# Optimization experiments

Measured on AMD Instinct MI355X. Metric: run time of the kernel, lower is better.

Reference implementation:

```python
import jax, jax.numpy as jnp
import numpy as np

NUM_ITERATIONS = 3
EPS = 1e-08

def squash(s, axis=-1):
    norm = jnp.linalg.norm(s, axis=axis, keepdims=True)
    scale = norm ** 2 / (1 + norm ** 2)
    return scale * s / (norm + EPS)

def setup_inputs() -> dict:
    key = jax.random.key(0)
    k1, k2 = jax.random.split(key)
    B, C, M, O, I = 256, 1152, 8, 16, 8
    u = jax.random.normal(k1, (B, C, I), dtype=jnp.float32)
    W = jax.random.normal(k2, (C, M, O, I), dtype=jnp.float32)
    return {"u": u, "W": W}

def reference(u, W):
    B, C, I = u.shape
    M, O = W.shape[1], W.shape[2]
    # u_hat: [B, C, M, O] -- predicted output capsule vectors
    u_hat = jnp.einsum('cmoi,bci->bcmo', W, u)
    b = jnp.zeros((B, C, M), dtype=u.dtype)
    v = None
    for r in range(NUM_ITERATIONS):
        c = jax.nn.softmax(b, axis=2)  # softmax over emotion dim
        s = jnp.einsum('bcm,bcmo->bmo', c, u_hat)
        v = squash(s)  # [B, M, O]
        if r < NUM_ITERATIONS - 1:
            uv = jnp.einsum('bcmo,bmo->bcm', u_hat, v)
            b = b + uv
    return v
```

## Files before the change

kernel.cpp:

```cpp
#include <hip/hip_runtime.h>

#define B_SZ 256
#define C_SZ 1152
#define MO   128
#define CSPL 32
#define CRNG (C_SZ / CSPL)
#define CAPS_EPS 1e-8f

struct alignas(8) H4 { _Float16 h[4]; };
union PK2 { unsigned int u32; _Float16 h[2]; };

__global__ __launch_bounds__(256) void caps_uhat(
    const float* __restrict__ u,
    const float* __restrict__ W,
    unsigned int* __restrict__ uhat)
{
    const int bid = blockIdx.x;
    const int c   = (bid & 7) * 144 + (bid >> 3);
    const int l   = threadIdx.x & 63;
    const int wv  = __builtin_amdgcn_readfirstlane(threadIdx.x >> 6);

    const float4* wp =
        reinterpret_cast<const float4*>(W + (size_t)c * 1024) + l * 4;
    const float4 wa = wp[0], wb = wp[1], wc4 = wp[2], wd = wp[3];

    unsigned int* ub = uhat + (size_t)c * B_SZ * 64 + l;
    const int b0 = wv * 64;

    for (int bb = 0; bb < 64; bb += 8) {
#pragma unroll
        for (int k = 0; k < 8; ++k) {
            const int b = b0 + bb + k;
            const float4* up = reinterpret_cast<const float4*>(
                u + ((size_t)b * C_SZ + c) * 8);
            const float4 u0 = up[0], u1 = up[1];
            float h0 = wa.x*u0.x + wa.y*u0.y + wa.z*u0.z + wa.w*u0.w
                     + wb.x*u1.x + wb.y*u1.y + wb.z*u1.z + wb.w*u1.w;
            float h1 = wc4.x*u0.x + wc4.y*u0.y + wc4.z*u0.z + wc4.w*u0.w
                     + wd.x*u1.x + wd.y*u1.y + wd.z*u1.z + wd.w*u1.w;
            PK2 pk;
            pk.h[0] = (_Float16)h0;
            pk.h[1] = (_Float16)h1;
            ub[(size_t)b * 64] = pk.u32;
        }
    }
}

__global__ __launch_bounds__(128) void caps_vcalc(
    const float* __restrict__ part_in,
    const float* __restrict__ addv,
    float* __restrict__ vout)
{
    const int b = blockIdx.x, t = threadIdx.x;
    float s = 0.f;
#pragma unroll
    for (int k = 0; k < CSPL; ++k)
        s += part_in[((size_t)k * B_SZ + b) * MO + t];
    float n2 = s * s;
    n2 += __shfl_xor(n2, 1);
    n2 += __shfl_xor(n2, 2);
    n2 += __shfl_xor(n2, 4);
    n2 += __shfl_xor(n2, 8);
    float norm = sqrtf(n2);
    float v = (n2 / (1.f + n2)) * s / (norm + CAPS_EPS);
    if (addv) v += addv[(size_t)b * MO + t];
    vout[(size_t)b * MO + t] = v;
}

template <bool UNIF>
__global__ __launch_bounds__(256) void caps_route(
    const H4* __restrict__ uhat,
    const float* __restrict__ vbuf,
    float* __restrict__ part_out)
{
    const int bt  = blockIdx.x & 31;
    const int csp = blockIdx.x >> 5;
    const int tid = threadIdx.x;
    const int g   = tid >> 5;
    const int l   = tid & 31;
    const int b   = bt * 8 + g;
    const int mo4 = l * 4;

    float4 v4 = make_float4(0.f, 0.f, 0.f, 0.f);
    if (!UNIF)
        v4 = *reinterpret_cast<const float4*>(vbuf + (size_t)b * MO + mo4);
    float acc[4] = {0.f, 0.f, 0.f, 0.f};

    const int cbeg = csp * CRNG, cend = cbeg + CRNG;
    const H4* base = uhat + (size_t)b * 32 + l;

    H4 r0 = base[(size_t)cbeg * B_SZ * 32];
    H4 r1 = base[(size_t)(cbeg + 1) * B_SZ * 32];

    for (int c = cbeg; c < cend; c += 2) {
        H4 n0 = r0, n1 = r1;
        if (c + 2 < cend) {
            n0 = base[(size_t)(c + 2) * B_SZ * 32];
            n1 = base[(size_t)(c + 3) * B_SZ * 32];
        }
#pragma unroll
        for (int q = 0; q < 2; ++q) {
            H4 r = q ? r1 : r0;
            float uh0 = (float)r.h[0], uh1 = (float)r.h[1];
            float uh2 = (float)r.h[2], uh3 = (float)r.h[3];
            float cw;
            if (UNIF) {
                cw = 0.125f;
            } else {
                float uv = uh0 * v4.x + uh1 * v4.y + uh2 * v4.z + uh3 * v4.w;
                uv += __shfl_xor(uv, 1);
                uv += __shfl_xor(uv, 2);
                float mx = fmaxf(uv, __shfl_xor(uv, 4));
                mx = fmaxf(mx, __shfl_xor(mx, 8));
                mx = fmaxf(mx, __shfl_xor(mx, 16));
                float e = expf(uv - mx);
                float den = e;
                den += __shfl_xor(den, 4);
                den += __shfl_xor(den, 8);
                den += __shfl_xor(den, 16);
                cw = e / den;
            }
            acc[0] = fmaf(cw, uh0, acc[0]);
            acc[1] = fmaf(cw, uh1, acc[1]);
            acc[2] = fmaf(cw, uh2, acc[2]);
            acc[3] = fmaf(cw, uh3, acc[3]);
        }
        r0 = n0; r1 = n1;
    }
    *reinterpret_cast<float4*>(part_out + ((size_t)csp * B_SZ + b) * MO + mo4) =
        make_float4(acc[0], acc[1], acc[2], acc[3]);
}

template <int R>
__global__ __launch_bounds__(256) void caps_small(
    const float* __restrict__ u, const float* __restrict__ W,
    const float* __restrict__ s_in, const float* __restrict__ v0_in,
    float* __restrict__ s_out, float* __restrict__ v0_out,
    float* __restrict__ out)
{
    const int b = blockIdx.x, tid = threadIdx.x;
    __shared__ float sh_v[8][17];
    __shared__ float sh_part[256][17];

    if (R >= 1) {
        if (tid < 128) {
            float val = s_in[b * 128 + tid];
            float n2 = val * val;
            n2 += __shfl_xor(n2, 1); n2 += __shfl_xor(n2, 2);
            n2 += __shfl_xor(n2, 4); n2 += __shfl_xor(n2, 8);
            float norm = sqrtf(n2);
            float v = (n2 / (1.f + n2)) * val / (norm + CAPS_EPS);
            int m = tid >> 4, o = tid & 15;
            if (R == 1) { v0_out[b * 128 + tid] = v; sh_v[m][o] = v; }
            else        { sh_v[m][o] = v + v0_in[b * 128 + tid]; }
        }
        __syncthreads();
    }
    const int c_local = tid >> 3, m = tid & 7;
    float s_acc[16];
#pragma unroll
    for (int o = 0; o < 16; ++o) s_acc[o] = 0.f;
    for (int cc = 0; cc < C_SZ; cc += 32) {
        const int c = cc + c_local;
        const float4* up = reinterpret_cast<const float4*>(
            u + (size_t)(b * C_SZ + c) * 8);
        float4 u0 = up[0], u1 = up[1];
        float u8[8] = {u0.x, u0.y, u0.z, u0.w, u1.x, u1.y, u1.z, u1.w};
        float uh[16];
        const float4* wp = reinterpret_cast<const float4*>(
            W + (size_t)((c * 8 + m) * 16) * 8);
#pragma unroll
        for (int o = 0; o < 16; ++o) {
            float4 w0 = wp[o * 2], w1 = wp[o * 2 + 1];
            uh[o] = w0.x * u8[0] + w0.y * u8[1] + w0.z * u8[2] + w0.w * u8[3] +
                    w1.x * u8[4] + w1.y * u8[5] + w1.z * u8[6] + w1.w * u8[7];
        }
        float cw;
        if (R == 0) cw = 0.125f;
        else {
            float uv = 0.f;
#pragma unroll
            for (int o = 0; o < 16; ++o) uv = fmaf(uh[o], sh_v[m][o], uv);
            float mx = uv;
            mx = fmaxf(mx, __shfl_xor(mx, 1));
            mx = fmaxf(mx, __shfl_xor(mx, 2));
            mx = fmaxf(mx, __shfl_xor(mx, 4));
            float e = expf(uv - mx);
            float den = e;
            den += __shfl_xor(den, 1); den += __shfl_xor(den, 2);
            den += __shfl_xor(den, 4);
            cw = e / den;
        }
#pragma unroll
        for (int o = 0; o < 16; ++o) s_acc[o] = fmaf(cw, uh[o], s_acc[o]);
    }
#pragma unroll
    for (int o = 0; o < 16; ++o) sh_part[tid][o] = s_acc[o];
    __syncthreads();
    if (tid < 128) {
        const int m2 = tid >> 4, o2 = tid & 15;
        float s = 0.f;
#pragma unroll
        for (int gg = 0; gg < 32; ++gg) s += sh_part[gg * 8 + m2][o2];
        if (R < 2) s_out[b * 128 + tid] = s;
        else {
            float n2 = s * s;
            n2 += __shfl_xor(n2, 1); n2 += __shfl_xor(n2, 2);
            n2 += __shfl_xor(n2, 4); n2 += __shfl_xor(n2, 8);
            float norm = sqrtf(n2);
            out[b * 128 + tid] = (n2 / (1.f + n2)) * s / (norm + CAPS_EPS);
        }
    }
}

extern "C" void kernel_launch(void* const* d_in, const int* in_sizes, int n_in,
                              void* d_out, int out_size, void* d_ws, size_t ws_size,
                              hipStream_t stream) {
    const float* u = (const float*)d_in[0];
    const float* W = (const float*)d_in[1];
    float* out = (float*)d_out;

    const size_t UHAT_BYTES  = (size_t)C_SZ * B_SZ * MO * 2;
    const size_t PART_FLOATS = (size_t)CSPL * B_SZ * MO;
    const size_t NEED = UHAT_BYTES + 2 * PART_FLOATS * 4 + 2 * B_SZ * MO * 4;

    if (ws_size >= NEED) {
        unsigned int* uhat_w = (unsigned int*)d_ws;
        const H4* uhat_r = (const H4*)d_ws;
        float* partA = (float*)((char*)d_ws + UHAT_BYTES);
        float* partB = partA + PART_FLOATS;
        float* v0    = partB + PART_FLOATS;
        float* vsum  = v0 + B_SZ * MO;

        dim3 gridU(C_SZ), gridR(CSPL * 32), blk(256);
        caps_uhat<<<gridU, blk, 0, stream>>>(u, W, uhat_w);
        caps_route<true ><<<gridR, blk, 0, stream>>>(uhat_r, nullptr, partA);
        caps_vcalc<<<dim3(B_SZ), dim3(128), 0, stream>>>(partA, nullptr, v0);
        caps_route<false><<<gridR, blk, 0, stream>>>(uhat_r, v0, partB);
        caps_vcalc<<<dim3(B_SZ), dim3(128), 0, stream>>>(partB, v0, vsum);
        caps_route<false><<<gridR, blk, 0, stream>>>(uhat_r, vsum, partA);
        caps_vcalc<<<dim3(B_SZ), dim3(128), 0, stream>>>(partA, nullptr, out);
    } else {
        float* sA = (float*)d_ws;
        float* sB = sA + 32768;
        float* v0 = sB + 32768;
        dim3 grid(B_SZ), blk(256);
        caps_small<0><<<grid, blk, 0, stream>>>(u, W, nullptr, nullptr, sA, nullptr, nullptr);
        caps_small<1><<<grid, blk, 0, stream>>>(u, W, sA, nullptr, sB, v0, nullptr);
        caps_small<2><<<grid, blk, 0, stream>>>(u, W, sB, v0, nullptr, nullptr, out);
    }
}
```

Measured before the change: 98.90 us.

## Stage W and u in LDS for u_hat kernel, write 16-byte packed outputs

Rewrites the u_hat producer so each block handles half the batch for one input capsule. W and u are staged in shared memory, and each thread keeps an 8x8 slice of W in registers to compute 8 outputs per batch element, which are stored as one 16-byte uint4. This replaces the per-lane 4-byte scattered stores and repeated global u loads. It raises register pressure and adds a barrier. The vcalc loop is no longer unrolled and the partial buffers are renamed, with three now allocated.

```diff
diff --git a/kernel.cpp b/kernel.cpp
--- a/kernel.cpp
+++ b/kernel.cpp
@@ -3,58 +3,83 @@
 #define B_SZ 256
 #define C_SZ 1152
 #define MO   128
+#define CAPS_EPS 1e-8f
+
 #define CSPL 32
 #define CRNG (C_SZ / CSPL)
-#define CAPS_EPS 1e-8f
 
 struct alignas(8) H4 { _Float16 h[4]; };
 union PK2 { unsigned int u32; _Float16 h[2]; };
 
-__global__ __launch_bounds__(256) void caps_uhat(
+__global__ __launch_bounds__(256, 4) void caps_uhat_w(
     const float* __restrict__ u,
     const float* __restrict__ W,
-    unsigned int* __restrict__ uhat)
-{
-    const int bid = blockIdx.x;
-    const int c   = (bid & 7) * 144 + (bid >> 3);
-    const int l   = threadIdx.x & 63;
-    const int wv  = __builtin_amdgcn_readfirstlane(threadIdx.x >> 6);
-
-    const float4* wp =
-        reinterpret_cast<const float4*>(W + (size_t)c * 1024) + l * 4;
-    const float4 wa = wp[0], wb = wp[1], wc4 = wp[2], wd = wp[3];
-
-    unsigned int* ub = uhat + (size_t)c * B_SZ * 64 + l;
-    const int b0 = wv * 64;
-
-    for (int bb = 0; bb < 64; bb += 8) {
-#pragma unroll
-        for (int k = 0; k < 8; ++k) {
-            const int b = b0 + bb + k;
-            const float4* up = reinterpret_cast<const float4*>(
-                u + ((size_t)b * C_SZ + c) * 8);
-            const float4 u0 = up[0], u1 = up[1];
-            float h0 = wa.x*u0.x + wa.y*u0.y + wa.z*u0.z + wa.w*u0.w
-                     + wb.x*u1.x + wb.y*u1.y + wb.z*u1.z + wb.w*u1.w;
-            float h1 = wc4.x*u0.x + wc4.y*u0.y + wc4.z*u0.z + wc4.w*u0.w
-                     + wd.x*u1.x + wd.y*u1.y + wd.z*u1.z + wd.w*u1.w;
-            PK2 pk;
-            pk.h[0] = (_Float16)h0;
-            pk.h[1] = (_Float16)h1;
-            ub[(size_t)b * 64] = pk.u32;
-        }
+    uint4* __restrict__ uhat)
+{
+    const int bid  = blockIdx.x;
+    const int c    = bid >> 1;
+    const int half = bid & 1;
+    const int tid  = threadIdx.x;
+    const int l    = tid & 63;
+    const int wv   = tid >> 6;
+    const int j    = l & 15;
+    const int bg   = l >> 4;
+
+    __shared__ __align__(16) float W_sh[1024];
+    __shared__ __align__(16) float u_sh[128][8];
+
+    *reinterpret_cast<float4*>(&W_sh[tid * 4]) =
+        *reinterpret_cast<const float4*>(W + (size_t)c * 1024 + tid * 4);
+    {
+        const int bl = tid >> 1, i0 = (tid & 1) * 4;
+        *reinterpret_cast<float4*>(&u_sh[bl][i0]) =
+            *reinterpret_cast<const float4*>(
+                u + ((size_t)(half * 128 + bl) * C_SZ + c) * 8 + i0);
+    }
+    __syncthreads();
+
+    float w[8][8];
+#pragma unroll
+    for (int r = 0; r < 8; ++r) {
+        const float4 a =
+            *reinterpret_cast<const float4*>(&W_sh[(j * 8 + r) * 8]);
+        const float4 b4 =
+            *reinterpret_cast<const float4*>(&W_sh[(j * 8 + r) * 8 + 4]);
+        w[r][0] = a.x;  w[r][1] = a.y;  w[r][2] = a.z;  w[r][3] = a.w;
+        w[r][4] = b4.x; w[r][5] = b4.y; w[r][6] = b4.z; w[r][7] = b4.w;
+    }
+
+    uint4* outp =
+        uhat + ((size_t)c * B_SZ + half * 128 + wv * 32 + bg) * 16 + j;
+
+#pragma unroll
+    for (int it = 0; it < 8; ++it) {
+        const int bl = wv * 32 + it * 4 + bg;
+        const float4 u0 = *reinterpret_cast<const float4*>(&u_sh[bl][0]);
+        const float4 u1 = *reinterpret_cast<const float4*>(&u_sh[bl][4]);
+        float h[8];
+#pragma unroll
+        for (int r = 0; r < 8; ++r)
+            h[r] = w[r][0]*u0.x + w[r][1]*u0.y + w[r][2]*u0.z + w[r][3]*u0.w
+                 + w[r][4]*u1.x + w[r][5]*u1.y + w[r][6]*u1.z + w[r][7]*u1.w;
+        PK2 p0, p1, p2, p3;
+        p0.h[0] = (_Float16)h[0]; p0.h[1] = (_Float16)h[1];
+        p1.h[0] = (_Float16)h[2]; p1.h[1] = (_Float16)h[3];
+        p2.h[0] = (_Float16)h[4]; p2.h[1] = (_Float16)h[5];
+        p3.h[0] = (_Float16)h[6]; p3.h[1] = (_Float16)h[7];
+        outp[(size_t)it * 64] = make_uint4(p0.u32, p1.u32, p2.u32, p3.u32);
     }
 }
 
 __global__ __launch_bounds__(128) void caps_vcalc(
     const float* __restrict__ part_in,
     const float* __restrict__ addv,
-    float* __restrict__ vout)
+    float* __restrict__ vout,
+    int nsplit)
 {
     const int b = blockIdx.x, t = threadIdx.x;
     float s = 0.f;
-#pragma unroll
-    for (int k = 0; k < CSPL; ++k)
+    for (int k = 0; k < nsplit; ++k)
         s += part_in[((size_t)k * B_SZ + b) * MO + t];
     float n2 = s * s;
     n2 += __shfl_xor(n2, 1);
@@ -220,26 +245,27 @@
     const float* W = (const float*)d_in[1];
     float* out = (float*)d_out;
 
-    const size_t UHAT_BYTES  = (size_t)C_SZ * B_SZ * MO * 2;
-    const size_t PART_FLOATS = (size_t)CSPL * B_SZ * MO;
-    const size_t NEED = UHAT_BYTES + 2 * PART_FLOATS * 4 + 2 * B_SZ * MO * 4;
+    const size_t UHAT_BYTES = (size_t)C_SZ * B_SZ * MO * 2;
+    const size_t PR_FLOATS  = (size_t)CSPL * B_SZ * MO;
+    const size_t NEED = UHAT_BYTES + (3 * PR_FLOATS + 2 * B_SZ * MO) * 4;
 
     if (ws_size >= NEED) {
-        unsigned int* uhat_w = (unsigned int*)d_ws;
+        uint4* uhat_w4   = (uint4*)d_ws;
         const H4* uhat_r = (const H4*)d_ws;
-        float* partA = (float*)((char*)d_ws + UHAT_BYTES);
-        float* partB = partA + PART_FLOATS;
-        float* v0    = partB + PART_FLOATS;
+        float* part0 = (float*)((char*)d_ws + UHAT_BYTES);
+        float* partA = part0 + PR_FLOATS;
+        float* partB = partA + PR_FLOATS;
+        float* v0    = partB + PR_FLOATS;
         float* vsum  = v0 + B_SZ * MO;
 
-        dim3 gridU(C_SZ), gridR(CSPL * 32), blk(256);
-        caps_uhat<<<gridU, blk, 0, stream>>>(u, W, uhat_w);
-        caps_route<true ><<<gridR, blk, 0, stream>>>(uhat_r, nullptr, partA);
-        caps_vcalc<<<dim3(B_SZ), dim3(128), 0, stream>>>(partA, nullptr, v0);
-        caps_route<false><<<gridR, blk, 0, stream>>>(uhat_r, v0, partB);
-        caps_vcalc<<<dim3(B_SZ), dim3(128), 0, stream>>>(partB, v0, vsum);
-        caps_route<false><<<gridR, blk, 0, stream>>>(uhat_r, vsum, partA);
-        caps_vcalc<<<dim3(B_SZ), dim3(128), 0, stream>>>(partA, nullptr, out);
+        dim3 blk(256);
+        caps_uhat_w<<<dim3(C_SZ * 2), blk, 0, stream>>>(u, W, uhat_w4);
+        caps_route<true ><<<dim3(CSPL * 32), blk, 0, stream>>>(uhat_r, nullptr, part0);
+        caps_vcalc<<<dim3(B_SZ), dim3(128), 0, stream>>>(part0, nullptr, v0, CSPL);
+        caps_route<false><<<dim3(CSPL * 32), blk, 0, stream>>>(uhat_r, v0, partA);
+        caps_vcalc<<<dim3(B_SZ), dim3(128), 0, stream>>>(partA, v0, vsum, CSPL);
+        caps_route<false><<<dim3(CSPL * 32), blk, 0, stream>>>(uhat_r, vsum, partB);
+        caps_vcalc<<<dim3(B_SZ), dim3(128), 0, stream>>>(partB, nullptr, out, CSPL);
     } else {
         float* sA = (float*)d_ws;
         float* sB = sA + 32768;
```

Result: slower. 119.1 us (+20.4%).
